# Kernel tuning notes

Measured on AMD Instinct MI355X. Metric: run time of the kernel, lower is better.

The kernel has to match this reference:

```python
import jax, jax.numpy as jnp
import numpy as np

B, S, H = 32, 8, 4096          # batch, new tokens, hidden
HQ, HK, D, L = 32, 8, 128, 4096  # q heads, kv heads, head_dim, max cache len
HALF = D // 2
W_STD = 0.02


def setup_inputs() -> dict:
    key = jax.random.key(0)
    ks = jax.random.split(key, 8)
    hidden_states = jax.random.normal(ks[0], (B, S, H), jnp.float32)
    past_key_value = jax.random.normal(ks[1], (2, B, L, HK, D), jnp.float32)
    rope_rotary_cos_sin = jax.random.uniform(ks[2], (B, S, 2, HALF), jnp.float32)
    context_lengths = jax.random.randint(ks[3], (B,), 0, L - S, dtype=jnp.int32)
    kvcache_start_index = context_lengths  # new tokens appended right after context
    Wq = jax.random.normal(ks[4], (HQ * D, H), jnp.float32) * W_STD
    Wk = jax.random.normal(ks[5], (HK * D, H), jnp.float32) * W_STD
    Wv = jax.random.normal(ks[6], (HK * D, H), jnp.float32) * W_STD
    Wo = jax.random.normal(ks[7], (H, HQ * D), jnp.float32) * W_STD
    return {
        'hidden_states': hidden_states,
        'past_key_value': past_key_value,
        'rope_rotary_cos_sin': rope_rotary_cos_sin,
        'context_lengths': context_lengths,
        'kvcache_start_index': kvcache_start_index,
        'Wq': Wq, 'Wk': Wk, 'Wv': Wv, 'Wo': Wo,
    }


def reference(hidden_states, past_key_value, rope_rotary_cos_sin,
              context_lengths, kvcache_start_index, Wq, Wk, Wv, Wo):
    # q/k/v projections (no bias)
    q = (hidden_states @ Wq.T).reshape(B, S, HQ, D)
    k = (hidden_states @ Wk.T).reshape(B, S, HK, D)
    v = (hidden_states @ Wv.T).reshape(B, S, HK, D)

    # inline RoPE (rotate-half, GPT-NeoX style) on q and k
    cos = rope_rotary_cos_sin[:, :, 0][:, :, None, :]  # [B,S,1,HALF]
    sin = rope_rotary_cos_sin[:, :, 1][:, :, None, :]

    def rot(x):
        x1, x2 = x[..., :HALF], x[..., HALF:]
        return jnp.concatenate([x1 * cos - x2 * sin, x2 * cos + x1 * sin], axis=-1)

    q = rot(q)
    k = rot(k)

    # write new k/v into the cache at kvcache_start_index (ragged per batch)
    b_idx = jnp.arange(B)[:, None]                                # [B,1]
    pos = kvcache_start_index[:, None] + jnp.arange(S)[None, :]   # [B,S]
    k_cache = past_key_value[0].at[b_idx, pos].set(k)             # [B,L,HK,D]
    v_cache = past_key_value[1].at[b_idx, pos].set(v)
    present_key_value = jnp.stack([k_cache, v_cache])

    # GQA attention: group 4 query heads per kv head
    G = HQ // HK
    qg = q.reshape(B, S, HK, G, D)
    scale = 1.0 / jnp.sqrt(jnp.asarray(D, q.dtype))
    scores = jnp.einsum('bshgd,blhd->bhgsl', qg, k_cache) * scale  # [B,HK,G,S,L]

    # causal mask over ragged context: key j visible iff j <= ctx_len + t
    q_pos = context_lengths[:, None, None] + jnp.arange(S)[None, :, None]  # [B,S,1]
    valid = jnp.arange(L)[None, None, :] <= q_pos                          # [B,S,L]
    scores = jnp.where(valid[:, None, None, :, :], scores,
                       jnp.finfo(scores.dtype).min)
    probs = jax.nn.softmax(scores, axis=-1)
    attn = jnp.einsum('bhgsl,blhd->bshgd', probs, v_cache).reshape(B, S, HQ * D)

    return attn @ Wo.T, present_key_value
```

## Files before the change

### kernel.cpp

```cpp
#include <hip/hip_runtime.h>

#define B_ 32
#define S_ 8
#define H_ 4096
#define HQ_ 32
#define HK_ 8
#define D_ 128
#define L_ 4096
#define KK 4096

typedef short s16x8 __attribute__((ext_vector_type(8)));
typedef float f32x4 __attribute__((ext_vector_type(4)));

static __device__ __forceinline__ unsigned short f2bf(float x){
  unsigned int u = __builtin_bit_cast(unsigned int, x);
  u += 0x7fffu + ((u >> 16) & 1u);
  return (unsigned short)(u >> 16);
}

static __device__ __forceinline__ s16x8 cvt8(f32x4 a, f32x4 b){
  s16x8 r;
  r[0]=(short)f2bf(a[0]); r[1]=(short)f2bf(a[1]); r[2]=(short)f2bf(a[2]); r[3]=(short)f2bf(a[3]);
  r[4]=(short)f2bf(b[0]); r[5]=(short)f2bf(b[1]); r[6]=(short)f2bf(b[2]); r[7]=(short)f2bf(b[3]);
  return r;
}

__global__ __launch_bounds__(256) void gemm_qkv(const float* __restrict__ A,
    const float* __restrict__ Wq, const float* __restrict__ Wk,
    const float* __restrict__ Wv, float* __restrict__ C)
{
  __shared__ short As[64][72];
  __shared__ short Bs[64][72];
  const int m0 = blockIdx.y * 64;
  const int n0 = blockIdx.x * 64;
  const float* W; int nw;
  if (n0 < 4096){ W = Wq; nw = n0; }
  else if (n0 < 5120){ W = Wk; nw = n0 - 4096; }
  else { W = Wv; nw = n0 - 5120; }
  const int tid = threadIdx.x;
  const int lane = tid & 63;
  const int w = tid >> 6;
  const int c = lane & 15;
  const int g = lane >> 4;
  const int wm = (w & 1) * 32;
  const int wn = (w >> 1) * 32;
  const int srow = tid >> 3;
  const int skc  = tid & 7;

  const float* Ar0 = A + (m0 + srow) * KK + skc * 8;
  const float* Ar1 = Ar0 + 32 * KK;
  const float* Wr0 = W + (nw + srow) * KK + skc * 8;
  const float* Wr1 = Wr0 + 32 * KK;

  f32x4 acc00 = {0.f,0.f,0.f,0.f};
  f32x4 acc01 = acc00, acc10 = acc00, acc11 = acc00;

  for (int kt = 0; kt < KK; kt += 64){
    __syncthreads();
    {
      f32x4 x0 = *(const f32x4*)(Ar0 + kt);
      f32x4 x1 = *(const f32x4*)(Ar0 + kt + 4);
      f32x4 x2 = *(const f32x4*)(Ar1 + kt);
      f32x4 x3 = *(const f32x4*)(Ar1 + kt + 4);
      f32x4 y0 = *(const f32x4*)(Wr0 + kt);
      f32x4 y1 = *(const f32x4*)(Wr0 + kt + 4);
      f32x4 y2 = *(const f32x4*)(Wr1 + kt);
      f32x4 y3 = *(const f32x4*)(Wr1 + kt + 4);
      *(s16x8*)&As[srow][skc*8]    = cvt8(x0, x1);
      *(s16x8*)&As[srow+32][skc*8] = cvt8(x2, x3);
      *(s16x8*)&Bs[srow][skc*8]    = cvt8(y0, y1);
      *(s16x8*)&Bs[srow+32][skc*8] = cvt8(y2, y3);
    }
    __syncthreads();
#pragma unroll
    for (int kk = 0; kk < 2; ++kk){
      s16x8 a0 = *(const s16x8*)&As[wm + c][kk*32 + 8*g];
      s16x8 a1 = *(const s16x8*)&As[wm + 16 + c][kk*32 + 8*g];
      s16x8 b0 = *(const s16x8*)&Bs[wn + c][kk*32 + 8*g];
      s16x8 b1 = *(const s16x8*)&Bs[wn + 16 + c][kk*32 + 8*g];
      acc00 = __builtin_amdgcn_mfma_f32_16x16x32_bf16(a0, b0, acc00, 0, 0, 0);
      acc01 = __builtin_amdgcn_mfma_f32_16x16x32_bf16(a0, b1, acc01, 0, 0, 0);
      acc10 = __builtin_amdgcn_mfma_f32_16x16x32_bf16(a1, b0, acc10, 0, 0, 0);
      acc11 = __builtin_amdgcn_mfma_f32_16x16x32_bf16(a1, b1, acc11, 0, 0, 0);
    }
  }
#pragma unroll
  for (int r = 0; r < 4; ++r){
    int row0 = m0 + wm + 4*g + r;
    int row1 = row0 + 16;
    int col0 = n0 + wn + c;
    int col1 = col0 + 16;
    C[row0 * 6144 + col0] = acc00[r];
    C[row0 * 6144 + col1] = acc01[r];
    C[row1 * 6144 + col0] = acc10[r];
    C[row1 * 6144 + col1] = acc11[r];
  }
}

__global__ __launch_bounds__(256) void gemm_bt(const float* __restrict__ A,
    const float* __restrict__ W, float* __restrict__ C, int N)
{
  __shared__ short As[64][72];
  __shared__ short Bs[64][72];
  const int m0 = blockIdx.y * 64;
  const int n0 = blockIdx.x * 64;
  const int tid = threadIdx.x;
  const int lane = tid & 63;
  const int w = tid >> 6;
  const int c = lane & 15;
  const int g = lane >> 4;
  const int wm = (w & 1) * 32;
  const int wn = (w >> 1) * 32;
  const int srow = tid >> 3;
  const int skc  = tid & 7;

  const float* Ar0 = A + (m0 + srow) * KK + skc * 8;
  const float* Ar1 = Ar0 + 32 * KK;
  const float* Wr0 = W + (n0 + srow) * KK + skc * 8;
  const float* Wr1 = Wr0 + 32 * KK;

  f32x4 acc00 = {0.f,0.f,0.f,0.f};
  f32x4 acc01 = acc00, acc10 = acc00, acc11 = acc00;

  for (int kt = 0; kt < KK; kt += 64){
    __syncthreads();
    {
      f32x4 x0 = *(const f32x4*)(Ar0 + kt);
      f32x4 x1 = *(const f32x4*)(Ar0 + kt + 4);
      f32x4 x2 = *(const f32x4*)(Ar1 + kt);
      f32x4 x3 = *(const f32x4*)(Ar1 + kt + 4);
      f32x4 y0 = *(const f32x4*)(Wr0 + kt);
      f32x4 y1 = *(const f32x4*)(Wr0 + kt + 4);
      f32x4 y2 = *(const f32x4*)(Wr1 + kt);
      f32x4 y3 = *(const f32x4*)(Wr1 + kt + 4);
      *(s16x8*)&As[srow][skc*8]    = cvt8(x0, x1);
      *(s16x8*)&As[srow+32][skc*8] = cvt8(x2, x3);
      *(s16x8*)&Bs[srow][skc*8]    = cvt8(y0, y1);
      *(s16x8*)&Bs[srow+32][skc*8] = cvt8(y2, y3);
    }
    __syncthreads();
#pragma unroll
    for (int kk = 0; kk < 2; ++kk){
      s16x8 a0 = *(const s16x8*)&As[wm + c][kk*32 + 8*g];
      s16x8 a1 = *(const s16x8*)&As[wm + 16 + c][kk*32 + 8*g];
      s16x8 b0 = *(const s16x8*)&Bs[wn + c][kk*32 + 8*g];
      s16x8 b1 = *(const s16x8*)&Bs[wn + 16 + c][kk*32 + 8*g];
      acc00 = __builtin_amdgcn_mfma_f32_16x16x32_bf16(a0, b0, acc00, 0, 0, 0);
      acc01 = __builtin_amdgcn_mfma_f32_16x16x32_bf16(a0, b1, acc01, 0, 0, 0);
      acc10 = __builtin_amdgcn_mfma_f32_16x16x32_bf16(a1, b0, acc10, 0, 0, 0);
      acc11 = __builtin_amdgcn_mfma_f32_16x16x32_bf16(a1, b1, acc11, 0, 0, 0);
    }
  }
#pragma unroll
  for (int r = 0; r < 4; ++r){
    int row0 = m0 + wm + 4*g + r;
    int row1 = row0 + 16;
    int col0 = n0 + wn + c;
    int col1 = col0 + 16;
    C[row0 * N + col0] = acc00[r];
    C[row0 * N + col1] = acc01[r];
    C[row1 * N + col0] = acc10[r];
    C[row1 * N + col1] = acc11[r];
  }
}

__global__ __launch_bounds__(256) void rope_prep(
    const float* __restrict__ qkv, const float* __restrict__ rope,
    unsigned short* __restrict__ qbuf, float* __restrict__ wskr, float* __restrict__ wsvc)
{
  const int bs = blockIdx.x;
  const int tid = threadIdx.x;
  const float* cosv = rope + bs * 128;
  const float* sinv = cosv + 64;
  const float* row = qkv + bs * 6144;
#pragma unroll
  for (int it = 0; it < 16; ++it){
    int e = tid + it * 256;
    int d = e & 127; int dh = d & 63;
    float x  = row[e];
    float xp = row[e ^ 64];
    float o = (d < 64) ? (x * cosv[dh] - xp * sinv[dh]) : (x * cosv[dh] + xp * sinv[dh]);
    qbuf[bs*4096 + e] = f2bf(o);
  }
#pragma unroll
  for (int it = 0; it < 4; ++it){
    int e = tid + it * 256;
    int d = e & 127; int dh = d & 63;
    float x  = row[4096 + e];
    float xp = row[4096 + (e ^ 64)];
    float o = (d < 64) ? (x * cosv[dh] - xp * sinv[dh]) : (x * cosv[dh] + xp * sinv[dh]);
    wskr[bs*1024 + e] = o;
    wsvc[bs*1024 + e] = row[5120 + e];
  }
}

__global__ __launch_bounds__(256) void copy_attn(
    const float* __restrict__ past, const float* __restrict__ wskr,
    const float* __restrict__ wsvc, const unsigned short* __restrict__ qb,
    const int* __restrict__ ctxlen, const int* __restrict__ startv,
    float* __restrict__ cache,
    float* __restrict__ pO, float* __restrict__ pM, float* __restrict__ pS)
{
  const int bid = blockIdx.x;
  const int sp = bid & 3;
  const int hk = (bid >> 2) & 7;
  const int b  = bid >> 5;
  const int tid = threadIdx.x;
  const int w = tid >> 6;
  const int lane = tid & 63;
  const int c = lane & 15;
  const int g = lane >> 4;
  const int ctx = ctxlen[b];
  const int pos = startv[b];
  const int lbase = sp * 1024;
  const int pid = bid * 4 + w;
  const float scale = 0.08838834764831845f;

  const float* Kpast = past + (size_t)b * 4194304 + hk * 128;
  const float* Vpast = Kpast + 134217728;
  float* Kout = cache + (size_t)b * 4194304 + hk * 128;
  float* Vout = Kout + 134217728;
  const float* KnewB = wskr + b * 8192 + hk * 128 - pos * 1024;
  const float* VnewB = wsvc + b * 8192 + hk * 128 - pos * 1024;

  s16x8 qf[2][4];
#pragma unroll
  for (int j = 0; j < 2; ++j){
    int r = j*16 + c; int s = r & 7; int gh = r >> 3;
    const unsigned short* qp = qb + (((b*8 + s) * 32) + hk*4 + gh) * 128 + 8*g;
#pragma unroll
    for (int ks = 0; ks < 4; ++ks)
      qf[j][ks] = __builtin_bit_cast(s16x8, *(const uint4*)(qp + ks*32));
  }

  f32x4 zero4 = {0.f,0.f,0.f,0.f};
  f32x4 accO[2][8];
#pragma unroll
  for (int i = 0; i < 2; ++i)
#pragma unroll
    for (int t = 0; t < 8; ++t) accO[i][t] = zero4;

  float m_j[2] = {-1e30f, -1e30f};
  float s_j[2] = {0.f, 0.f};

  for (int ci = w; ci < 32; ci += 4){
    const int l0 = lbase + ci * 32;
    if (l0 > ctx + 7){
      const int r = lane >> 5;
      const int fq = lane & 31;
#pragma unroll
      for (int j = 0; j < 16; ++j){
        int row = l0 + r + 2*j;
        bool kn = ((unsigned)(row - pos)) < 8u;
        const f32x4* kp = (const f32x4*)((kn ? KnewB : Kpast) + row*1024) + fq;
        const f32x4* vp = (const f32x4*)((kn ? VnewB : Vpast) + row*1024) + fq;
        f32x4 kv = __builtin_nontemporal_load(kp);
        f32x4 vv = __builtin_nontemporal_load(vp);
        __builtin_nontemporal_store(kv, (f32x4*)(Kout + row*1024) + fq);
        __builtin_nontemporal_store(vv, (f32x4*)(Vout + row*1024) + fq);
      }
      continue;
    }
    s16x8 kf[2][4];
#pragma unroll
    for (int i = 0; i < 2; ++i){
      int row = l0 + i*16 + c;
      bool kn = ((unsigned)(row - pos)) < 8u;
      const float* src = (kn ? KnewB : Kpast) + row*1024 + 8*g;
      float* dst = Kout + row*1024 + 8*g;
#pragma unroll
      for (int ks = 0; ks < 4; ++ks){
        f32x4 x = *(const f32x4*)(src + ks*32);
        f32x4 y = *(const f32x4*)(src + ks*32 + 4);
        __builtin_nontemporal_store(x, (f32x4*)(dst + ks*32));
        __builtin_nontemporal_store(y, (f32x4*)(dst + ks*32 + 4));
        kf[i][ks] = cvt8(x, y);
      }
    }
    f32x4 sc[2][2];
#pragma unroll
    for (int i = 0; i < 2; ++i)
#pragma unroll
      for (int j = 0; j < 2; ++j) sc[i][j] = zero4;
#pragma unroll
    for (int ks = 0; ks < 4; ++ks)
#pragma unroll
      for (int i = 0; i < 2; ++i)
#pragma unroll
        for (int j = 0; j < 2; ++j)
          sc[i][j] = __builtin_amdgcn_mfma_f32_16x16x32_bf16(kf[i][ks], qf[j][ks], sc[i][j], 0, 0, 0);

    float p[2][2][4];
    float fj[2];
#pragma unroll
    for (int j = 0; j < 2; ++j){
      const int qpos = ctx + ((j*16 + c) & 7);
      float mx = -1e30f;
#pragma unroll
      for (int i = 0; i < 2; ++i)
#pragma unroll
        for (int r = 0; r < 4; ++r){
          int lg = l0 + i*16 + 4*g + r;
          float v = (lg <= qpos) ? sc[i][j][r] * scale : -1e30f;
          p[i][j][r] = v;
          mx = fmaxf(mx, v);
        }
      mx = fmaxf(mx, __shfl_xor(mx, 16));
      mx = fmaxf(mx, __shfl_xor(mx, 32));
      float mnew = fmaxf(m_j[j], mx);
      float f = __expf(m_j[j] - mnew);
      float lsum = 0.f;
#pragma unroll
      for (int i = 0; i < 2; ++i)
#pragma unroll
        for (int r = 0; r < 4; ++r){
          int lg = l0 + i*16 + 4*g + r;
          float pv = (lg <= qpos) ? __expf(p[i][j][r] - mnew) : 0.f;
          p[i][j][r] = pv;
          lsum += pv;
        }
      s_j[j] = s_j[j] * f + lsum;
      m_j[j] = mnew;
      fj[j] = f;
    }
#pragma unroll
    for (int iq = 0; iq < 2; ++iq)
#pragma unroll
      for (int r = 0; r < 4; ++r){
        float fo = __shfl(fj[iq], 4*g + r);
#pragma unroll
        for (int t = 0; t < 8; ++t) accO[iq][t][r] *= fo;
      }
    s16x8 pf[2];
#pragma unroll
    for (int iq = 0; iq < 2; ++iq){
      int pd00 = (int)((unsigned)f2bf(p[0][iq][0]) | ((unsigned)f2bf(p[0][iq][1]) << 16));
      int pd01 = (int)((unsigned)f2bf(p[0][iq][2]) | ((unsigned)f2bf(p[0][iq][3]) << 16));
      int pd10 = (int)((unsigned)f2bf(p[1][iq][0]) | ((unsigned)f2bf(p[1][iq][1]) << 16));
      int pd11 = (int)((unsigned)f2bf(p[1][iq][2]) | ((unsigned)f2bf(p[1][iq][3]) << 16));
      int sA = (((2*g) & 3) << 4) | c;
      int sB = (((2*g + 1) & 3) << 4) | c;
      int h = g >> 1;
      int t0a = __shfl(pd00, sA), t1a = __shfl(pd10, sA);
      int t0b = __shfl(pd01, sA), t1b = __shfl(pd11, sA);
      int t0c = __shfl(pd00, sB), t1c = __shfl(pd10, sB);
      int t0d = __shfl(pd01, sB), t1d = __shfl(pd11, sB);
      int4 dw;
      dw.x = h ? t1a : t0a;
      dw.y = h ? t1b : t0b;
      dw.z = h ? t1c : t0c;
      dw.w = h ? t1d : t0d;
      pf[iq] = __builtin_bit_cast(s16x8, dw);
    }
#pragma unroll
    for (int t = 0; t < 8; ++t){
      const int co = t*16 + c;
      float vv[8];
#pragma unroll
      for (int jj = 0; jj < 8; ++jj){
        int row = l0 + 8*g + jj;
        bool kn = ((unsigned)(row - pos)) < 8u;
        float x = *((kn ? VnewB : Vpast) + row*1024 + co);
        __builtin_nontemporal_store(x, Vout + row*1024 + co);
        vv[jj] = x;
      }
      f32x4 va, vb;
      va[0] = vv[0]; va[1] = vv[1]; va[2] = vv[2]; va[3] = vv[3];
      vb[0] = vv[4]; vb[1] = vv[5]; vb[2] = vv[6]; vb[3] = vv[7];
      s16x8 vf = cvt8(va, vb);
      accO[0][t] = __builtin_amdgcn_mfma_f32_16x16x32_bf16(pf[0], vf, accO[0][t], 0, 0, 0);
      accO[1][t] = __builtin_amdgcn_mfma_f32_16x16x32_bf16(pf[1], vf, accO[1][t], 0, 0, 0);
    }
  }
#pragma unroll
  for (int j = 0; j < 2; ++j){
    float sj = s_j[j];
    sj += __shfl_xor(sj, 16);
    sj += __shfl_xor(sj, 32);
    if (g == 0){
      pM[pid*32 + j*16 + c] = m_j[j];
      pS[pid*32 + j*16 + c] = sj;
    }
  }
#pragma unroll
  for (int iq = 0; iq < 2; ++iq)
#pragma unroll
    for (int t = 0; t < 8; ++t)
#pragma unroll
      for (int r = 0; r < 4; ++r)
        pO[(pid*32 + iq*16 + 4*g + r) * 128 + t*16 + c] = accO[iq][t][r];
}

__global__ __launch_bounds__(256) void merge_attn(const float* __restrict__ pO,
    const float* __restrict__ pM, const float* __restrict__ pS, float* __restrict__ attn)
{
  const int bh = blockIdx.x;
  const int b = bh >> 3, hk = bh & 7;
  const int tid = threadIdx.x;
  const int q = tid >> 3;
  const int d0 = (tid & 7) * 16;
  const int base = bh * 16;
  float eP[16];
  float M = -1e30f;
#pragma unroll
  for (int p2 = 0; p2 < 16; ++p2){
    float m = pM[(base + p2) * 32 + q];
    eP[p2] = m;
    M = fmaxf(M, m);
  }
  float den = 0.f;
#pragma unroll
  for (int p2 = 0; p2 < 16; ++p2){
    float e = __expf(eP[p2] - M);
    eP[p2] = e;
    den += e * pS[(base + p2) * 32 + q];
  }
  float inv = 1.f / den;
  float a[16];
#pragma unroll
  for (int k2 = 0; k2 < 16; ++k2) a[k2] = 0.f;
#pragma unroll
  for (int p2 = 0; p2 < 16; ++p2){
    const float* src = pO + ((base + p2) * 32 + q) * 128 + d0;
    float e = eP[p2];
    f32x4 v0 = *(const f32x4*)(src);
    f32x4 v1 = *(const f32x4*)(src + 4);
    f32x4 v2 = *(const f32x4*)(src + 8);
    f32x4 v3 = *(const f32x4*)(src + 12);
    a[0]  += e * v0[0]; a[1]  += e * v0[1]; a[2]  += e * v0[2]; a[3]  += e * v0[3];
    a[4]  += e * v1[0]; a[5]  += e * v1[1]; a[6]  += e * v1[2]; a[7]  += e * v1[3];
    a[8]  += e * v2[0]; a[9]  += e * v2[1]; a[10] += e * v2[2]; a[11] += e * v2[3];
    a[12] += e * v3[0]; a[13] += e * v3[1]; a[14] += e * v3[2]; a[15] += e * v3[3];
  }
  const int gh = q >> 3, s = q & 7;
  float* o = attn + (b*8 + s) * 4096 + (hk*4 + gh) * 128 + d0;
#pragma unroll
  for (int k2 = 0; k2 < 16; ++k2) o[k2] = a[k2] * inv;
}

extern "C" void kernel_launch(void* const* d_in, const int* in_sizes, int n_in,
                              void* d_out, int out_size, void* d_ws, size_t ws_size,
                              hipStream_t stream) {
  const float* hidden = (const float*)d_in[0];
  const float* past   = (const float*)d_in[1];
  const float* rope   = (const float*)d_in[2];
  const int*   ctx    = (const int*)d_in[3];
  const int*   start  = (const int*)d_in[4];
  const float* Wq     = (const float*)d_in[5];
  const float* Wk     = (const float*)d_in[6];
  const float* Wv     = (const float*)d_in[7];
  const float* Wo     = (const float*)d_in[8];

  float* out_attn  = (float*)d_out;
  float* out_cache = out_attn + 1048576;

  float* ws = (float*)d_ws;
  float* qkv    = ws;
  float* wsattn = ws + 1572864;
  float* wskr   = wsattn;
  float* wsvc   = wsattn + 262144;
  unsigned short* qb = (unsigned short*)(ws + 2621440);
  float* pO = ws + 3145728;
  float* pM = ws + 19922944;
  float* pS = ws + 20054016;

  gemm_qkv<<<dim3(96, 4), 256, 0, stream>>>(hidden, Wq, Wk, Wv, qkv);

  rope_prep<<<256, 256, 0, stream>>>(qkv, rope, qb, wskr, wsvc);

  copy_attn<<<1024, 256, 0, stream>>>(past, wskr, wsvc, qb, ctx, start,
                                      out_cache, pO, pM, pS);
  merge_attn<<<B_ * HK_, 256, 0, stream>>>(pO, pM, pS, wsattn);

  gemm_bt<<<dim3(64, 4), 256, 0, stream>>>(wsattn, Wo, out_attn, 4096);
}
```

Baseline: 709.4 us.

## Enlarge GEMM M-tile to 128 and coalesce cache copy in attention

Both projection GEMMs now compute a 128x64 output tile per block instead of 64x64, so each weight tile is loaded and converted once for twice as many rows. This halves weight-matrix traffic at the cost of half as many blocks (192 and 128) on a large GPU, which lowers occupancy. In the attention kernel, the K/V cache copy for active chunks now goes through a separate row-contiguous, fully coalesced float4 loop instead of scattered scalar stores interleaved with the MFMA loads. This makes the writes coalesced but reads each K/V chunk twice.

```diff
diff --git a/kernel.cpp b/kernel.cpp
--- a/kernel.cpp
+++ b/kernel.cpp
@@ -29,9 +29,9 @@
     const float* __restrict__ Wq, const float* __restrict__ Wk,
     const float* __restrict__ Wv, float* __restrict__ C)
 {
-  __shared__ short As[64][72];
+  __shared__ short As[128][72];
   __shared__ short Bs[64][72];
-  const int m0 = blockIdx.y * 64;
+  const int m0 = blockIdx.y * 128;
   const int n0 = blockIdx.x * 64;
   const float* W; int nw;
   if (n0 < 4096){ W = Wq; nw = n0; }
@@ -47,62 +47,76 @@
   const int srow = tid >> 3;
   const int skc  = tid & 7;
 
-  const float* Ar0 = A + (m0 + srow) * KK + skc * 8;
-  const float* Ar1 = Ar0 + 32 * KK;
-  const float* Wr0 = W + (nw + srow) * KK + skc * 8;
-  const float* Wr1 = Wr0 + 32 * KK;
-
-  f32x4 acc00 = {0.f,0.f,0.f,0.f};
-  f32x4 acc01 = acc00, acc10 = acc00, acc11 = acc00;
+  const float* Arp = A + (m0 + srow) * KK + skc * 8;
+  const float* Wrp = W + (nw + srow) * KK + skc * 8;
+
+  f32x4 zero4 = {0.f,0.f,0.f,0.f};
+  f32x4 acc[2][2][2];
+#pragma unroll
+  for (int mh = 0; mh < 2; ++mh)
+#pragma unroll
+    for (int mi = 0; mi < 2; ++mi)
+#pragma unroll
+      for (int ni = 0; ni < 2; ++ni) acc[mh][mi][ni] = zero4;
 
   for (int kt = 0; kt < KK; kt += 64){
     __syncthreads();
     {
-      f32x4 x0 = *(const f32x4*)(Ar0 + kt);
-      f32x4 x1 = *(const f32x4*)(Ar0 + kt + 4);
-      f32x4 x2 = *(const f32x4*)(Ar1 + kt);
-      f32x4 x3 = *(const f32x4*)(Ar1 + kt + 4);
-      f32x4 y0 = *(const f32x4*)(Wr0 + kt);
-      f32x4 y1 = *(const f32x4*)(Wr0 + kt + 4);
-      f32x4 y2 = *(const f32x4*)(Wr1 + kt);
-      f32x4 y3 = *(const f32x4*)(Wr1 + kt + 4);
-      *(s16x8*)&As[srow][skc*8]    = cvt8(x0, x1);
-      *(s16x8*)&As[srow+32][skc*8] = cvt8(x2, x3);
-      *(s16x8*)&Bs[srow][skc*8]    = cvt8(y0, y1);
-      *(s16x8*)&Bs[srow+32][skc*8] = cvt8(y2, y3);
+      f32x4 xa0 = *(const f32x4*)(Arp + 0*32*KK + kt);
+      f32x4 xb0 = *(const f32x4*)(Arp + 0*32*KK + kt + 4);
+      f32x4 xa1 = *(const f32x4*)(Arp + 1*32*KK + kt);
+      f32x4 xb1 = *(const f32x4*)(Arp + 1*32*KK + kt + 4);
+      f32x4 xa2 = *(const f32x4*)(Arp + 2*32*KK + kt);
+      f32x4 xb2 = *(const f32x4*)(Arp + 2*32*KK + kt + 4);
+      f32x4 xa3 = *(const f32x4*)(Arp + 3*32*KK + kt);
+      f32x4 xb3 = *(const f32x4*)(Arp + 3*32*KK + kt + 4);
+      f32x4 ya0 = *(const f32x4*)(Wrp + 0*32*KK + kt);
+      f32x4 yb0 = *(const f32x4*)(Wrp + 0*32*KK + kt + 4);
+      f32x4 ya1 = *(const f32x4*)(Wrp + 1*32*KK + kt);
+      f32x4 yb1 = *(const f32x4*)(Wrp + 1*32*KK + kt + 4);
+      *(s16x8*)&As[srow      ][skc*8] = cvt8(xa0, xb0);
+      *(s16x8*)&As[srow + 32 ][skc*8] = cvt8(xa1, xb1);
+      *(s16x8*)&As[srow + 64 ][skc*8] = cvt8(xa2, xb2);
+      *(s16x8*)&As[srow + 96 ][skc*8] = cvt8(xa3, xb3);
+      *(s16x8*)&Bs[srow      ][skc*8] = cvt8(ya0, yb0);
+      *(s16x8*)&Bs[srow + 32 ][skc*8] = cvt8(ya1, yb1);
     }
     __syncthreads();
 #pragma unroll
     for (int kk = 0; kk < 2; ++kk){
-      s16x8 a0 = *(const s16x8*)&As[wm + c][kk*32 + 8*g];
-      s16x8 a1 = *(const s16x8*)&As[wm + 16 + c][kk*32 + 8*g];
       s16x8 b0 = *(const s16x8*)&Bs[wn + c][kk*32 + 8*g];
       s16x8 b1 = *(const s16x8*)&Bs[wn + 16 + c][kk*32 + 8*g];
-      acc00 = __builtin_amdgcn_mfma_f32_16x16x32_bf16(a0, b0, acc00, 0, 0, 0);
-      acc01 = __builtin_amdgcn_mfma_f32_16x16x32_bf16(a0, b1, acc01, 0, 0, 0);
-      acc10 = __builtin_amdgcn_mfma_f32_16x16x32_bf16(a1, b0, acc10, 0, 0, 0);
-      acc11 = __builtin_amdgcn_mfma_f32_16x16x32_bf16(a1, b1, acc11, 0, 0, 0);
-    }
-  }
-#pragma unroll
-  for (int r = 0; r < 4; ++r){
-    int row0 = m0 + wm + 4*g + r;
-    int row1 = row0 + 16;
-    int col0 = n0 + wn + c;
-    int col1 = col0 + 16;
-    C[row0 * 6144 + col0] = acc00[r];
-    C[row0 * 6144 + col1] = acc01[r];
-    C[row1 * 6144 + col0] = acc10[r];
-    C[row1 * 6144 + col1] = acc11[r];
-  }
+#pragma unroll
+      for (int mh = 0; mh < 2; ++mh){
+        s16x8 a0 = *(const s16x8*)&As[mh*64 + wm + c][kk*32 + 8*g];
+        s16x8 a1 = *(const s16x8*)&As[mh*64 + wm + 16 + c][kk*32 + 8*g];
+        acc[mh][0][0] = __builtin_amdgcn_mfma_f32_16x16x32_bf16(a0, b0, acc[mh][0][0], 0, 0, 0);
+        acc[mh][0][1] = __builtin_amdgcn_mfma_f32_16x16x32_bf16(a0, b1, acc[mh][0][1], 0, 0, 0);
+        acc[mh][1][0] = __builtin_amdgcn_mfma_f32_16x16x32_bf16(a1, b0, acc[mh][1][0], 0, 0, 0);
+        acc[mh][1][1] = __builtin_amdgcn_mfma_f32_16x16x32_bf16(a1, b1, acc[mh][1][1], 0, 0, 0);
+      }
+    }
+  }
+#pragma unroll
+  for (int mh = 0; mh < 2; ++mh)
+#pragma unroll
+    for (int mi = 0; mi < 2; ++mi)
+#pragma unroll
+      for (int ni = 0; ni < 2; ++ni)
+#pragma unroll
+        for (int r = 0; r < 4; ++r){
+          int row = m0 + mh*64 + wm + mi*16 + 4*g + r;
+          int col = n0 + wn + ni*16 + c;
+          C[row * 6144 + col] = acc[mh][mi][ni][r];
+        }
 }
 
 __global__ __launch_bounds__(256) void gemm_bt(const float* __restrict__ A,
     const float* __restrict__ W, float* __restrict__ C, int N)
 {
-  __shared__ short As[64][72];
+  __shared__ short As[128][72];
   __shared__ short Bs[64][72];
-  const int m0 = blockIdx.y * 64;
+  const int m0 = blockIdx.y * 128;
   const int n0 = blockIdx.x * 64;
   const int tid = threadIdx.x;
   const int lane = tid & 63;
@@ -114,54 +128,68 @@
   const int srow = tid >> 3;
   const int skc  = tid & 7;
 
-  const float* Ar0 = A + (m0 + srow) * KK + skc * 8;
-  const float* Ar1 = Ar0 + 32 * KK;
-  const float* Wr0 = W + (n0 + srow) * KK + skc * 8;
-  const float* Wr1 = Wr0 + 32 * KK;
-
-  f32x4 acc00 = {0.f,0.f,0.f,0.f};
-  f32x4 acc01 = acc00, acc10 = acc00, acc11 = acc00;
+  const float* Arp = A + (m0 + srow) * KK + skc * 8;
+  const float* Wrp = W + (n0 + srow) * KK + skc * 8;
+
+  f32x4 zero4 = {0.f,0.f,0.f,0.f};
+  f32x4 acc[2][2][2];
+#pragma unroll
+  for (int mh = 0; mh < 2; ++mh)
+#pragma unroll
+    for (int mi = 0; mi < 2; ++mi)
+#pragma unroll
+      for (int ni = 0; ni < 2; ++ni) acc[mh][mi][ni] = zero4;
 
   for (int kt = 0; kt < KK; kt += 64){
     __syncthreads();
     {
-      f32x4 x0 = *(const f32x4*)(Ar0 + kt);
-      f32x4 x1 = *(const f32x4*)(Ar0 + kt + 4);
-      f32x4 x2 = *(const f32x4*)(Ar1 + kt);
-      f32x4 x3 = *(const f32x4*)(Ar1 + kt + 4);
-      f32x4 y0 = *(const f32x4*)(Wr0 + kt);
-      f32x4 y1 = *(const f32x4*)(Wr0 + kt + 4);
-      f32x4 y2 = *(const f32x4*)(Wr1 + kt);
-      f32x4 y3 = *(const f32x4*)(Wr1 + kt + 4);
-      *(s16x8*)&As[srow][skc*8]    = cvt8(x0, x1);
-      *(s16x8*)&As[srow+32][skc*8] = cvt8(x2, x3);
-      *(s16x8*)&Bs[srow][skc*8]    = cvt8(y0, y1);
-      *(s16x8*)&Bs[srow+32][skc*8] = cvt8(y2, y3);
+      f32x4 xa0 = *(const f32x4*)(Arp + 0*32*KK + kt);
+      f32x4 xb0 = *(const f32x4*)(Arp + 0*32*KK + kt + 4);
+      f32x4 xa1 = *(const f32x4*)(Arp + 1*32*KK + kt);
+      f32x4 xb1 = *(const f32x4*)(Arp + 1*32*KK + kt + 4);
+      f32x4 xa2 = *(const f32x4*)(Arp + 2*32*KK + kt);
+      f32x4 xb2 = *(const f32x4*)(Arp + 2*32*KK + kt + 4);
+      f32x4 xa3 = *(const f32x4*)(Arp + 3*32*KK + kt);
+      f32x4 xb3 = *(const f32x4*)(Arp + 3*32*KK + kt + 4);
+      f32x4 ya0 = *(const f32x4*)(Wrp + 0*32*KK + kt);
+      f32x4 yb0 = *(const f32x4*)(Wrp + 0*32*KK + kt + 4);
+      f32x4 ya1 = *(const f32x4*)(Wrp + 1*32*KK + kt);
+      f32x4 yb1 = *(const f32x4*)(Wrp + 1*32*KK + kt + 4);
+      *(s16x8*)&As[srow      ][skc*8] = cvt8(xa0, xb0);
+      *(s16x8*)&As[srow + 32 ][skc*8] = cvt8(xa1, xb1);
+      *(s16x8*)&As[srow + 64 ][skc*8] = cvt8(xa2, xb2);
+      *(s16x8*)&As[srow + 96 ][skc*8] = cvt8(xa3, xb3);
+      *(s16x8*)&Bs[srow      ][skc*8] = cvt8(ya0, yb0);
+      *(s16x8*)&Bs[srow + 32 ][skc*8] = cvt8(ya1, yb1);
     }
     __syncthreads();
 #pragma unroll
     for (int kk = 0; kk < 2; ++kk){
-      s16x8 a0 = *(const s16x8*)&As[wm + c][kk*32 + 8*g];
-      s16x8 a1 = *(const s16x8*)&As[wm + 16 + c][kk*32 + 8*g];
       s16x8 b0 = *(const s16x8*)&Bs[wn + c][kk*32 + 8*g];
       s16x8 b1 = *(const s16x8*)&Bs[wn + 16 + c][kk*32 + 8*g];
-      acc00 = __builtin_amdgcn_mfma_f32_16x16x32_bf16(a0, b0, acc00, 0, 0, 0);
-      acc01 = __builtin_amdgcn_mfma_f32_16x16x32_bf16(a0, b1, acc01, 0, 0, 0);
-      acc10 = __builtin_amdgcn_mfma_f32_16x16x32_bf16(a1, b0, acc10, 0, 0, 0);
-      acc11 = __builtin_amdgcn_mfma_f32_16x16x32_bf16(a1, b1, acc11, 0, 0, 0);
-    }
-  }
-#pragma unroll
-  for (int r = 0; r < 4; ++r){
-    int row0 = m0 + wm + 4*g + r;
-    int row1 = row0 + 16;
-    int col0 = n0 + wn + c;
-    int col1 = col0 + 16;
-    C[row0 * N + col0] = acc00[r];
-    C[row0 * N + col1] = acc01[r];
-    C[row1 * N + col0] = acc10[r];
-    C[row1 * N + col1] = acc11[r];
-  }
+#pragma unroll
+      for (int mh = 0; mh < 2; ++mh){
+        s16x8 a0 = *(const s16x8*)&As[mh*64 + wm + c][kk*32 + 8*g];
+        s16x8 a1 = *(const s16x8*)&As[mh*64 + wm + 16 + c][kk*32 + 8*g];
+        acc[mh][0][0] = __builtin_amdgcn_mfma_f32_16x16x32_bf16(a0, b0, acc[mh][0][0], 0, 0, 0);
+        acc[mh][0][1] = __builtin_amdgcn_mfma_f32_16x16x32_bf16(a0, b1, acc[mh][0][1], 0, 0, 0);
+        acc[mh][1][0] = __builtin_amdgcn_mfma_f32_16x16x32_bf16(a1, b0, acc[mh][1][0], 0, 0, 0);
+        acc[mh][1][1] = __builtin_amdgcn_mfma_f32_16x16x32_bf16(a1, b1, acc[mh][1][1], 0, 0, 0);
+      }
+    }
+  }
+#pragma unroll
+  for (int mh = 0; mh < 2; ++mh)
+#pragma unroll
+    for (int mi = 0; mi < 2; ++mi)
+#pragma unroll
+      for (int ni = 0; ni < 2; ++ni)
+#pragma unroll
+        for (int r = 0; r < 4; ++r){
+          int row = m0 + mh*64 + wm + mi*16 + 4*g + r;
+          int col = n0 + wn + ni*16 + c;
+          C[row * N + col] = acc[mh][mi][ni][r];
+        }
 }
 
 __global__ __launch_bounds__(256) void rope_prep(
@@ -243,14 +271,15 @@
   float m_j[2] = {-1e30f, -1e30f};
   float s_j[2] = {0.f, 0.f};
 
+  const int rr = lane >> 5;
+  const int fq = lane & 31;
+
   for (int ci = w; ci < 32; ci += 4){
     const int l0 = lbase + ci * 32;
     if (l0 > ctx + 7){
-      const int r = lane >> 5;
-      const int fq = lane & 31;
 #pragma unroll
       for (int j = 0; j < 16; ++j){
-        int row = l0 + r + 2*j;
+        int row = l0 + rr + 2*j;
         bool kn = ((unsigned)(row - pos)) < 8u;
         const f32x4* kp = (const f32x4*)((kn ? KnewB : Kpast) + row*1024) + fq;
         const f32x4* vp = (const f32x4*)((kn ? VnewB : Vpast) + row*1024) + fq;
@@ -261,19 +290,25 @@
       }
       continue;
     }
+#pragma unroll
+    for (int j = 0; j < 16; ++j){
+      int row = l0 + rr + 2*j;
+      bool kn = ((unsigned)(row - pos)) < 8u;
+      f32x4 kv = *((const f32x4*)((kn ? KnewB : Kpast) + row*1024) + fq);
+      f32x4 vv = *((const f32x4*)((kn ? VnewB : Vpast) + row*1024) + fq);
+      __builtin_nontemporal_store(kv, (f32x4*)(Kout + row*1024) + fq);
+      __builtin_nontemporal_store(vv, (f32x4*)(Vout + row*1024) + fq);
+    }
     s16x8 kf[2][4];
 #pragma unroll
     for (int i = 0; i < 2; ++i){
       int row = l0 + i*16 + c;
       bool kn = ((unsigned)(row - pos)) < 8u;
       const float* src = (kn ? KnewB : Kpast) + row*1024 + 8*g;
-      float* dst = Kout + row*1024 + 8*g;
 #pragma unroll
       for (int ks = 0; ks < 4; ++ks){
         f32x4 x = *(const f32x4*)(src + ks*32);
         f32x4 y = *(const f32x4*)(src + ks*32 + 4);
-        __builtin_nontemporal_store(x, (f32x4*)(dst + ks*32));
-        __builtin_nontemporal_store(y, (f32x4*)(dst + ks*32 + 4));
         kf[i][ks] = cvt8(x, y);
       }
     }
@@ -360,9 +395,7 @@
       for (int jj = 0; jj < 8; ++jj){
         int row = l0 + 8*g + jj;
         bool kn = ((unsigned)(row - pos)) < 8u;
-        float x = *((kn ? VnewB : Vpast) + row*1024 + co);
-        __builtin_nontemporal_store(x, Vout + row*1024 + co);
-        vv[jj] = x;
+        vv[jj] = *((kn ? VnewB : Vpast) + row*1024 + co);
       }
       f32x4 va, vb;
       va[0] = vv[0]; va[1] = vv[1]; va[2] = vv[2]; va[3] = vv[3];
@@ -464,7 +497,7 @@
   float* pM = ws + 19922944;
   float* pS = ws + 20054016;
 
-  gemm_qkv<<<dim3(96, 4), 256, 0, stream>>>(hidden, Wq, Wk, Wv, qkv);
+  gemm_qkv<<<dim3(96, 2), 256, 0, stream>>>(hidden, Wq, Wk, Wv, qkv);
 
   rope_prep<<<256, 256, 0, stream>>>(qkv, rope, qb, wskr, wsvc);
 
@@ -472,5 +505,5 @@
                                       out_cache, pO, pM, pS);
   merge_attn<<<B_ * HK_, 256, 0, stream>>>(pO, pM, pS, wsattn);
 
-  gemm_bt<<<dim3(64, 4), 256, 0, stream>>>(wsattn, Wo, out_attn, 4096);
-}
+  gemm_bt<<<dim3(64, 2), 256, 0, stream>>>(wsattn, Wo, out_attn, 4096);
+}
```

Result: slower. 732.8 us (+3.3%).
